# Performance work log

Measured on AMD Instinct MI355X. Metric: run time of the kernel, lower is better.

Reference implementation:

```python
import jax, jax.numpy as jnp
import numpy as np

EPS = 1e-5  # torch LayerNorm default

def layernorm(x, gamma, beta):
    mu = jnp.mean(x, axis=-1, keepdims=True)
    var = jnp.mean(jnp.square(x - mu), axis=-1, keepdims=True)
    return (x - mu) * jax.lax.rsqrt(var + EPS) * gamma + beta

def setup_inputs() -> dict:
    key = jax.random.key(0)
    ks = jax.random.split(key, 8)
    B, S, D = 4, 2048, 1024
    s = 1.0 / np.sqrt(D)  # torch Linear init scale
    return {
        "x": jax.random.normal(ks[0], (B, S, D), dtype=jnp.float32),
        "Wq": jax.random.uniform(ks[1], (D, D), jnp.float32, -s, s),
        "bq": jax.random.uniform(ks[2], (D,), jnp.float32, -s, s),
        "Wk": jax.random.uniform(ks[3], (D, D), jnp.float32, -s, s),
        "bk": jax.random.uniform(ks[4], (D,), jnp.float32, -s, s),
        "Wv": jax.random.uniform(ks[5], (D, D), jnp.float32, -s, s),
        "bv": jax.random.uniform(ks[6], (D,), jnp.float32, -s, s),
        "gamma": jnp.ones((D,), jnp.float32),
        "beta": jnp.zeros((D,), jnp.float32),
    }

def reference(x, Wq, bq, Wk, bk, Wv, bv, gamma, beta):
    # torch Linear: x @ W.T + b; shared LayerNorm applied to each projection
    q = layernorm(jnp.einsum('bsd,ed->bse', x, Wq) + bq, gamma, beta)
    k = layernorm(jnp.einsum('bsd,ed->bse', x, Wk) + bk, gamma, beta)
    v = layernorm(jnp.einsum('bsd,ed->bse', x, Wv) + bv, gamma, beta)
    att = jnp.einsum('bqd,bkd->bqk', q, k)  # no 1/sqrt(d) scaling in original
    att = jax.nn.softmax(att, axis=-1)
    # dropout is identity in eval mode (reference baseline)
    return jnp.einsum('bqk,bkd->bqd', att, v)
```

## Files before the change

kernel.cpp:

```cpp
#include <hip/hip_runtime.h>

typedef _Float16 f16;
typedef __attribute__((ext_vector_type(4))) _Float16 f16x4;
typedef __attribute__((ext_vector_type(8))) _Float16 f16x8;
typedef __attribute__((ext_vector_type(4))) float f32x4;

#define GLB_AS __attribute__((address_space(1)))
#define LDS_AS __attribute__((address_space(3)))

__device__ __forceinline__ void async_copy16(const void* g, void* l) {
  __builtin_amdgcn_global_load_lds((const GLB_AS void*)g, (LDS_AS void*)l, 16, 0, 0);
}

#define WAITVM(N) asm volatile("s_waitcnt vmcnt(" #N ")" ::: "memory")
#define WAITLGKM0() asm volatile("s_waitcnt lgkmcnt(0)" ::: "memory")

#define STAGE_A(t_) do {                                                     \
    const int _b = (t_) & 3; const long _k = (long)(t_) * 32;                \
    async_copy16(Ag + _k, &Ash[_b][sl]);                                     \
    if constexpr (IA == 2)                                                   \
      async_copy16(Ag + _k + 128l * lda, &Ash[_b][sl + 128 * 32]);           \
  } while (0)
#define STAGE_B(t_) do {                                                     \
    const int _b = (t_) & 3; const long _k = (long)(t_) * 32;                \
    async_copy16(Bg + _k, &Bsh[_b][sl]);                                     \
    if constexpr (IB == 2)                                                   \
      async_copy16(Bg + _k + 128l * ldb, &Bsh[_b][sl + 128 * 32]);           \
  } while (0)

template <int BM, int BN, typename OutT, int MODE, bool BIAS>
__global__ __launch_bounds__(512, 2) void gemm8p(
    const f16* __restrict__ A, const f16* __restrict__ B, OutT* __restrict__ C,
    int lda, int ldb, int ldc, int K, long sA, long sB, long sC,
    int tiles_x, int tiles_y,
    const float* __restrict__ b0, const float* __restrict__ b1,
    const float* __restrict__ b2)
{
  constexpr int BK = 32;
  constexpr int WM = BM / 2, WN = BN / 4;
  constexpr int RM = WM / 16, RN = WN / 16;
  constexpr int IA = BM / 128, IB = BN / 128;
  constexpr int IT = IA + IB;

  __shared__ __align__(16) f16 Ash[4][BM * BK];
  __shared__ __align__(16) f16 Bsh[4][BN * BK];

  int bx, by, bz;
  {
    const int n = blockIdx.x;
    if (MODE == 0) {
      by = n % tiles_y;
      const int r = n / tiles_y;
      bx = r % tiles_x;
      bz = r / tiles_x;
    } else {
      const int j = n & 7, i = n >> 3, th = tiles_y >> 1;
      bz = j >> 1;
      bx = i / th;
      by = (j & 1) * th + i % th;
    }
  }

  A += (long)bz * sA;
  B += (long)bz * sB;
  C += (long)bz * sC;

  const int tid  = threadIdx.x;
  const int wave = tid >> 6, lane = tid & 63;
  const int wr = wave >> 2, wc = wave & 3;
  const int m0 = by * BM, n0 = bx * BN;
  const int r16 = lane & 15, quad = lane >> 4;

  const int srow = wave * 16 + (lane >> 2);
  const int schunk = ((lane & 3) ^ ((lane >> 3) & 3)) * 8;
  const f16* Ag = A + (long)(m0 + srow) * lda + schunk;
  const f16* Bg = B + (long)(n0 + srow) * ldb + schunk;
  const int sl = (wave * 16) * BK;

  const int NT = K / BK;

  STAGE_A(0); STAGE_B(0);
  STAGE_A(1); STAGE_B(1);
  STAGE_A(2); STAGE_B(2);

  f32x4 acc[RM][RN] = {};

  const int rchunk = (quad ^ ((r16 >> 1) & 3)) * 8;
  const int rdA = (wr * WM + r16) * BK + rchunk;
  const int rdB = (wc * WN + r16) * BK + rchunk;

  for (int t = 0; t < NT; ++t) {
    if constexpr (IT == 4) {
      if (t < NT - 2) { WAITVM(8); } else if (t == NT - 2) { WAITVM(4); } else { WAITVM(0); }
    } else {
      if (t < NT - 2) { WAITVM(6); } else if (t == NT - 2) { WAITVM(3); } else { WAITVM(0); }
    }
    __builtin_amdgcn_s_barrier();

    const f16* As = Ash[t & 3];
    const f16* Bs = Bsh[t & 3];
    f16x8 af[4], bf[RN];

    if constexpr (RM == 8) {
#pragma unroll
      for (int j = 0; j < RN; j++) bf[j] = *(const f16x8*)&Bs[rdB + j * 16 * BK];
#pragma unroll
      for (int i = 0; i < 4; i++) af[i] = *(const f16x8*)&As[rdA + i * 16 * BK];
      if (t + 3 < NT) STAGE_A(t + 3);
      __builtin_amdgcn_s_barrier();
      WAITLGKM0();
      __builtin_amdgcn_sched_barrier(0);
      __builtin_amdgcn_s_setprio(1);
#pragma unroll
      for (int i = 0; i < 4; i++)
#pragma unroll
        for (int j = 0; j < RN; j++)
          acc[i][j] = __builtin_amdgcn_mfma_f32_16x16x32_f16(af[i], bf[j], acc[i][j], 0, 0, 0);
      __builtin_amdgcn_s_setprio(0);
      __builtin_amdgcn_sched_barrier(0);
      __builtin_amdgcn_s_barrier();
      f16x8 af1[4];
#pragma unroll
      for (int i = 0; i < 4; i++) af1[i] = *(const f16x8*)&As[rdA + (4 + i) * 16 * BK];
      if (t + 3 < NT) STAGE_B(t + 3);
      __builtin_amdgcn_s_barrier();
      WAITLGKM0();
      __builtin_amdgcn_sched_barrier(0);
      __builtin_amdgcn_s_setprio(1);
#pragma unroll
      for (int i = 0; i < 4; i++)
#pragma unroll
        for (int j = 0; j < RN; j++)
          acc[4 + i][j] = __builtin_amdgcn_mfma_f32_16x16x32_f16(af1[i], bf[j], acc[4 + i][j], 0, 0, 0);
      __builtin_amdgcn_s_setprio(0);
      __builtin_amdgcn_sched_barrier(0);
    } else {
#pragma unroll
      for (int i = 0; i < 4; i++) af[i] = *(const f16x8*)&As[rdA + i * 16 * BK];
#pragma unroll
      for (int j = 0; j < 2; j++) bf[j] = *(const f16x8*)&Bs[rdB + j * 16 * BK];
      if (t + 3 < NT) STAGE_A(t + 3);
      __builtin_amdgcn_s_barrier();
      WAITLGKM0();
      __builtin_amdgcn_sched_barrier(0);
      __builtin_amdgcn_s_setprio(1);
#pragma unroll
      for (int i = 0; i < 4; i++)
#pragma unroll
        for (int j = 0; j < 2; j++)
          acc[i][j] = __builtin_amdgcn_mfma_f32_16x16x32_f16(af[i], bf[j], acc[i][j], 0, 0, 0);
      __builtin_amdgcn_s_setprio(0);
      __builtin_amdgcn_sched_barrier(0);
      __builtin_amdgcn_s_barrier();
#pragma unroll
      for (int j = 2; j < 4; j++) bf[j] = *(const f16x8*)&Bs[rdB + j * 16 * BK];
      if (t + 3 < NT) STAGE_B(t + 3);
      __builtin_amdgcn_s_barrier();
      WAITLGKM0();
      __builtin_amdgcn_sched_barrier(0);
      __builtin_amdgcn_s_setprio(1);
#pragma unroll
      for (int i = 0; i < 4; i++)
#pragma unroll
        for (int j = 2; j < 4; j++)
          acc[i][j] = __builtin_amdgcn_mfma_f32_16x16x32_f16(af[i], bf[j], acc[i][j], 0, 0, 0);
      __builtin_amdgcn_s_setprio(0);
      __builtin_amdgcn_sched_barrier(0);
    }
  }

  float bias_j[RN];
#pragma unroll
  for (int j = 0; j < RN; j++) bias_j[j] = 0.f;
  if constexpr (BIAS) {
    const float* bias = (bz == 0) ? b0 : (bz == 1) ? b1 : b2;
#pragma unroll
    for (int j = 0; j < RN; j++) bias_j[j] = bias[n0 + wc * WN + j * 16 + r16];
  }
#pragma unroll
  for (int i = 0; i < RM; i++)
#pragma unroll
    for (int j = 0; j < RN; j++)
#pragma unroll
      for (int r = 0; r < 4; r++) {
        long row = m0 + wr * WM + i * 16 + quad * 4 + r;
        long col = n0 + wc * WN + j * 16 + r16;
        C[row * (long)ldc + col] = (OutT)(acc[i][j][r] + bias_j[j]);
      }
}

__global__ __launch_bounds__(256) void cast_all(
    const float* __restrict__ x, const float* __restrict__ Wq,
    const float* __restrict__ Wk, const float* __restrict__ Wv,
    f16* __restrict__ Xh, f16* __restrict__ Wh)
{
  const long off = (long)blockIdx.x * 1024 + threadIdx.x * 4;
  const float* src;
  f16* dst;
  if (off < 8388608L) {
    src = x + off;
    dst = Xh + off;
  } else {
    const long o = off - 8388608L;
    src = (o < 1048576L) ? Wq + o
        : (o < 2097152L) ? Wk + (o - 1048576L)
                         : Wv + (o - 2097152L);
    dst = Wh + o;
  }
  const float4 v = *(const float4*)src;
  f16x4 h;
  h.x = (f16)v.x; h.y = (f16)v.y; h.z = (f16)v.z; h.w = (f16)v.w;
  *(f16x4*)dst = h;
}

__global__ __launch_bounds__(256) void ln_kernel(
    f16* __restrict__ P, const float* __restrict__ gamma,
    const float* __restrict__ beta)
{
  f16* p = P + (long)blockIdx.y * 8388608 + (long)blockIdx.x * 1024;
  const int tid = threadIdx.x;
  const int e = tid * 4;

  f16x4 raw = *(const f16x4*)(p + e);
  float v0 = (float)raw.x, v1 = (float)raw.y;
  float v2 = (float)raw.z, v3 = (float)raw.w;
  float s  = v0 + v1 + v2 + v3;
  float s2 = v0 * v0 + v1 * v1 + v2 * v2 + v3 * v3;

#pragma unroll
  for (int off = 32; off > 0; off >>= 1) {
    s  += __shfl_down(s, off, 64);
    s2 += __shfl_down(s2, off, 64);
  }
  __shared__ float red[10];
  const int wave = tid >> 6, lane = tid & 63;
  if (lane == 0) { red[wave] = s; red[4 + wave] = s2; }
  __syncthreads();
  if (tid == 0) {
    red[8] = red[0] + red[1] + red[2] + red[3];
    red[9] = red[4] + red[5] + red[6] + red[7];
  }
  __syncthreads();
  const float mu   = red[8] * (1.f / 1024.f);
  const float var  = red[9] * (1.f / 1024.f) - mu * mu;
  const float rstd = rsqrtf(var + 1e-5f);

  float4 gg = *(const float4*)(gamma + e);
  float4 be = *(const float4*)(beta + e);
  f16x4 o;
  o.x = (f16)((v0 - mu) * rstd * gg.x + be.x);
  o.y = (f16)((v1 - mu) * rstd * gg.y + be.y);
  o.z = (f16)((v2 - mu) * rstd * gg.z + be.z);
  o.w = (f16)((v3 - mu) * rstd * gg.w + be.w);
  *(f16x4*)(p + e) = o;
}

__global__ __launch_bounds__(256) void transpose_kernel(const f16* __restrict__ V,
                                                        f16* __restrict__ Vt)
{
  const int S = 2048, D = 1024;
  const f16* v = V + (long)blockIdx.z * ((long)S * D);
  f16* vt = Vt + (long)blockIdx.z * ((long)D * S);
  __shared__ f16 tile[64][66];
  const int d0 = blockIdx.x * 64, j0 = blockIdx.y * 64;
  const int tx = threadIdx.x & 63, ty = threadIdx.x >> 6;
#pragma unroll
  for (int r = ty; r < 64; r += 4)
    tile[r][tx] = v[(long)(j0 + r) * D + d0 + tx];
  __syncthreads();
#pragma unroll
  for (int r = ty; r < 64; r += 4)
    vt[(long)(d0 + r) * S + j0 + tx] = tile[tx][r];
}

__global__ __launch_bounds__(256) void softmax_kernel(float* __restrict__ Sc)
{
  float* srow = Sc + (long)blockIdx.x * 2048;
  const int tid = threadIdx.x;
  float4 a = ((const float4*)srow)[tid];
  float4 b = ((const float4*)srow)[256 + tid];

  float m = fmaxf(fmaxf(fmaxf(a.x, a.y), fmaxf(a.z, a.w)),
                  fmaxf(fmaxf(b.x, b.y), fmaxf(b.z, b.w)));
#pragma unroll
  for (int off = 32; off > 0; off >>= 1) m = fmaxf(m, __shfl_down(m, off, 64));
  __shared__ float red[6];
  const int wave = tid >> 6, lane = tid & 63;
  if (lane == 0) red[wave] = m;
  __syncthreads();
  if (tid == 0) red[4] = fmaxf(fmaxf(red[0], red[1]), fmaxf(red[2], red[3]));
  __syncthreads();
  const float M = red[4];

  a.x = __expf(a.x - M); a.y = __expf(a.y - M);
  a.z = __expf(a.z - M); a.w = __expf(a.w - M);
  b.x = __expf(b.x - M); b.y = __expf(b.y - M);
  b.z = __expf(b.z - M); b.w = __expf(b.w - M);
  float s = a.x + a.y + a.z + a.w + b.x + b.y + b.z + b.w;
#pragma unroll
  for (int off = 32; off > 0; off >>= 1) s += __shfl_down(s, off, 64);
  if (lane == 0) red[wave] = s;
  __syncthreads();
  if (tid == 0) red[5] = red[0] + red[1] + red[2] + red[3];
  __syncthreads();
  const float inv = 1.0f / red[5];

  f16* orow = (f16*)srow;
  f16x4 oa, ob;
  oa.x = (f16)(a.x * inv); oa.y = (f16)(a.y * inv);
  oa.z = (f16)(a.z * inv); oa.w = (f16)(a.w * inv);
  ob.x = (f16)(b.x * inv); ob.y = (f16)(b.y * inv);
  ob.z = (f16)(b.z * inv); ob.w = (f16)(b.w * inv);
  ((f16x4*)orow)[tid]       = oa;
  ((f16x4*)orow)[256 + tid] = ob;
}

extern "C" void kernel_launch(void* const* d_in, const int* in_sizes, int n_in,
                              void* d_out, int out_size, void* d_ws, size_t ws_size,
                              hipStream_t stream)
{
  const float* x     = (const float*)d_in[0];
  const float* Wq    = (const float*)d_in[1];
  const float* bq    = (const float*)d_in[2];
  const float* Wk    = (const float*)d_in[3];
  const float* bk    = (const float*)d_in[4];
  const float* Wv    = (const float*)d_in[5];
  const float* bv    = (const float*)d_in[6];
  const float* gamma = (const float*)d_in[7];
  const float* beta  = (const float*)d_in[8];
  float* out = (float*)d_out;

  char* ws = (char*)d_ws;
  f16*   P  = (f16*)(ws);
  f16*   Vt = (f16*)(ws + (48u << 20));
  float* Sc = (float*)(ws + (64u << 20));
  f16*   Xh = (f16*)(ws + (64u << 20));
  f16*   Wh = (f16*)(ws + (80u << 20));

  cast_all<<<11264, 256, 0, stream>>>(x, Wq, Wk, Wv, Xh, Wh);

  gemm8p<128, 256, f16, 0, true><<<768, 512, 0, stream>>>(
      Xh, Wh, P, 1024, 1024, 1024, 1024, 0L, 1048576L, 8388608L,
      4, 64, bq, bk, bv);

  ln_kernel<<<dim3(8192, 3), 256, 0, stream>>>(P, gamma, beta);

  transpose_kernel<<<dim3(16, 32, 4), 256, 0, stream>>>(P + 2L * 8388608, Vt);

  gemm8p<256, 256, float, 1, false><<<256, 512, 0, stream>>>(
      P, P + 8388608, Sc, 1024, 1024, 2048, 1024, 2097152L, 2097152L, 4194304L,
      8, 8, nullptr, nullptr, nullptr);

  softmax_kernel<<<8192, 256, 0, stream>>>(Sc);

  gemm8p<128, 256, float, 1, false><<<256, 512, 0, stream>>>(
      (const f16*)Sc, Vt, out, 4096, 2048, 1024, 2048, 8388608L, 2097152L, 2097152L,
      4, 16, nullptr, nullptr, nullptr);
}
```

Before: 305.0 us.

## Restructure GEMM mainloop to double-buffered BK=64 with split half-tile staging

Replaces the 4-stage BK=32 ring buffer with a 2-stage buffer of 64-wide K tiles. Each tile is stored as two 32-wide halves, and each half is staged asynchronously while the other half is consumed. It also changes the LDS swizzle pattern to a three-way XOR to reduce bank conflicts, and restricts the template to BN=256. The intent is fewer barriers and waits per unit of K and better overlap of global-to-LDS copies with MFMA work. The cost is a shallower prefetch distance, a more complex wait-count schedule and a narrower supported configuration.

```diff
diff --git a/kernel.cpp b/kernel.cpp
--- a/kernel.cpp
+++ b/kernel.cpp
@@ -14,18 +14,20 @@
 
 #define WAITVM(N) asm volatile("s_waitcnt vmcnt(" #N ")" ::: "memory")
 #define WAITLGKM0() asm volatile("s_waitcnt lgkmcnt(0)" ::: "memory")
-
-#define STAGE_A(t_) do {                                                     \
-    const int _b = (t_) & 3; const long _k = (long)(t_) * 32;                \
-    async_copy16(Ag + _k, &Ash[_b][sl]);                                     \
-    if constexpr (IA == 2)                                                   \
-      async_copy16(Ag + _k + 128l * lda, &Ash[_b][sl + 128 * 32]);           \
+#define BAR() __builtin_amdgcn_s_barrier()
+#define SB0() __builtin_amdgcn_sched_barrier(0)
+
+#define STAGE_A(t_, kk_) do {                                                \
+    const long _k = (long)(t_) * 64 + (kk_) * 32;                            \
+    f16* _d = &Ash[(t_) & 1][kk_][w16 * 32];                                 \
+    async_copy16(Ag + _k, _d);                                               \
+    if constexpr (IA == 2) async_copy16(Ag + _k + 128l * lda, _d + 4096);    \
   } while (0)
-#define STAGE_B(t_) do {                                                     \
-    const int _b = (t_) & 3; const long _k = (long)(t_) * 32;                \
-    async_copy16(Bg + _k, &Bsh[_b][sl]);                                     \
-    if constexpr (IB == 2)                                                   \
-      async_copy16(Bg + _k + 128l * ldb, &Bsh[_b][sl + 128 * 32]);           \
+#define STAGE_B(t_, kk_) do {                                                \
+    const long _k = (long)(t_) * 64 + (kk_) * 32;                            \
+    f16* _d = &Bsh[(t_) & 1][kk_][w16 * 32];                                 \
+    async_copy16(Bg + _k, _d);                                               \
+    async_copy16(Bg + _k + 128l * ldb, _d + 4096);                           \
   } while (0)
 
 template <int BM, int BN, typename OutT, int MODE, bool BIAS>
@@ -36,14 +38,13 @@
     const float* __restrict__ b0, const float* __restrict__ b1,
     const float* __restrict__ b2)
 {
-  constexpr int BK = 32;
   constexpr int WM = BM / 2, WN = BN / 4;
   constexpr int RM = WM / 16, RN = WN / 16;
-  constexpr int IA = BM / 128, IB = BN / 128;
-  constexpr int IT = IA + IB;
-
-  __shared__ __align__(16) f16 Ash[4][BM * BK];
-  __shared__ __align__(16) f16 Bsh[4][BN * BK];
+  constexpr int IA = BM / 128;
+  static_assert(RN == 4 && BN == 256, "template assumes BN=256");
+
+  __shared__ __align__(16) f16 Ash[2][2][BM * 32];
+  __shared__ __align__(16) f16 Bsh[2][2][BN * 32];
 
   int bx, by, bz;
   {
@@ -70,102 +71,127 @@
   const int wr = wave >> 2, wc = wave & 3;
   const int m0 = by * BM, n0 = bx * BN;
   const int r16 = lane & 15, quad = lane >> 4;
-
-  const int srow = wave * 16 + (lane >> 2);
-  const int schunk = ((lane & 3) ^ ((lane >> 3) & 3)) * 8;
-  const f16* Ag = A + (long)(m0 + srow) * lda + schunk;
-  const f16* Bg = B + (long)(n0 + srow) * ldb + schunk;
-  const int sl = (wave * 16) * BK;
-
-  const int NT = K / BK;
-
-  STAGE_A(0); STAGE_B(0);
-  STAGE_A(1); STAGE_B(1);
-  STAGE_A(2); STAGE_B(2);
+  const int w16 = wave * 16;
+
+  const int cg8 = (((lane & 3) ^ ((lane >> 2) & 3) ^ ((lane >> 4) & 3)) * 8);
+  const f16* Ag = A + (long)(m0 + w16 + (lane >> 2)) * lda + cg8;
+  const f16* Bg = B + (long)(n0 + w16 + (lane >> 2)) * ldb + cg8;
+
+  const int NT = K / 64;
+
+  STAGE_A(0, 0); STAGE_B(0, 0);
+  STAGE_A(0, 1); STAGE_B(0, 1);
+  STAGE_A(1, 0); STAGE_B(1, 0);
 
   f32x4 acc[RM][RN] = {};
 
-  const int rchunk = (quad ^ ((r16 >> 1) & 3)) * 8;
-  const int rdA = (wr * WM + r16) * BK + rchunk;
-  const int rdB = (wc * WN + r16) * BK + rchunk;
+  const int rc  = (quad ^ ((r16 ^ (r16 >> 2)) & 3)) * 8;
+  const int rdA = (wr * WM + r16) * 32 + rc;
+  const int rdB = (wc * WN + r16) * 32 + rc;
+
+  if constexpr (RM == 8) { WAITVM(8); } else { WAITVM(6); }
+  BAR();
 
   for (int t = 0; t < NT; ++t) {
-    if constexpr (IT == 4) {
-      if (t < NT - 2) { WAITVM(8); } else if (t == NT - 2) { WAITVM(4); } else { WAITVM(0); }
+    const int bp = t & 1;
+    const f16* A0 = &Ash[bp][0][0];
+    const f16* A1 = &Ash[bp][1][0];
+    const f16* B0 = &Bsh[bp][0][0];
+    const f16* B1 = &Bsh[bp][1][0];
+    f16x8 af[4], bf[4];
+
+    if constexpr (RM == 4) {
+#pragma unroll
+      for (int i = 0; i < 4; i++) af[i] = *(const f16x8*)&A0[rdA + i * 512];
+#pragma unroll
+      for (int j = 0; j < 4; j++) bf[j] = *(const f16x8*)&B0[rdB + j * 512];
+      if (t + 1 < NT) { STAGE_A(t + 1, 1); STAGE_B(t + 1, 1); }
+      BAR();
+      WAITLGKM0(); SB0();
+      __builtin_amdgcn_s_setprio(1);
+#pragma unroll
+      for (int i = 0; i < 4; i++)
+#pragma unroll
+        for (int j = 0; j < 4; j++)
+          acc[i][j] = __builtin_amdgcn_mfma_f32_16x16x32_f16(af[i], bf[j], acc[i][j], 0, 0, 0);
+      __builtin_amdgcn_s_setprio(0); SB0();
+      if (t < NT - 1) { WAITVM(6); } else { WAITVM(0); }
+      BAR();
+#pragma unroll
+      for (int i = 0; i < 4; i++) af[i] = *(const f16x8*)&A1[rdA + i * 512];
+#pragma unroll
+      for (int j = 0; j < 4; j++) bf[j] = *(const f16x8*)&B1[rdB + j * 512];
+      if (t + 2 < NT) { STAGE_A(t + 2, 0); STAGE_B(t + 2, 0); }
+      BAR();
+      WAITLGKM0(); SB0();
+      __builtin_amdgcn_s_setprio(1);
+#pragma unroll
+      for (int i = 0; i < 4; i++)
+#pragma unroll
+        for (int j = 0; j < 4; j++)
+          acc[i][j] = __builtin_amdgcn_mfma_f32_16x16x32_f16(af[i], bf[j], acc[i][j], 0, 0, 0);
+      __builtin_amdgcn_s_setprio(0); SB0();
+      if (t < NT - 2) { WAITVM(6); } else if (t == NT - 2) { WAITVM(3); } else { WAITVM(0); }
+      BAR();
     } else {
-      if (t < NT - 2) { WAITVM(6); } else if (t == NT - 2) { WAITVM(3); } else { WAITVM(0); }
-    }
-    __builtin_amdgcn_s_barrier();
-
-    const f16* As = Ash[t & 3];
-    const f16* Bs = Bsh[t & 3];
-    f16x8 af[4], bf[RN];
-
-    if constexpr (RM == 8) {
-#pragma unroll
-      for (int j = 0; j < RN; j++) bf[j] = *(const f16x8*)&Bs[rdB + j * 16 * BK];
-#pragma unroll
-      for (int i = 0; i < 4; i++) af[i] = *(const f16x8*)&As[rdA + i * 16 * BK];
-      if (t + 3 < NT) STAGE_A(t + 3);
-      __builtin_amdgcn_s_barrier();
-      WAITLGKM0();
-      __builtin_amdgcn_sched_barrier(0);
-      __builtin_amdgcn_s_setprio(1);
-#pragma unroll
-      for (int i = 0; i < 4; i++)
-#pragma unroll
-        for (int j = 0; j < RN; j++)
+#pragma unroll
+      for (int i = 0; i < 4; i++) af[i] = *(const f16x8*)&A0[rdA + i * 512];
+#pragma unroll
+      for (int j = 0; j < 4; j++) bf[j] = *(const f16x8*)&B0[rdB + j * 512];
+      if (t + 1 < NT) STAGE_A(t + 1, 1);
+      BAR();
+      WAITLGKM0(); SB0();
+      __builtin_amdgcn_s_setprio(1);
+#pragma unroll
+      for (int i = 0; i < 4; i++)
+#pragma unroll
+        for (int j = 0; j < 4; j++)
           acc[i][j] = __builtin_amdgcn_mfma_f32_16x16x32_f16(af[i], bf[j], acc[i][j], 0, 0, 0);
-      __builtin_amdgcn_s_setprio(0);
-      __builtin_amdgcn_sched_barrier(0);
-      __builtin_amdgcn_s_barrier();
-      f16x8 af1[4];
-#pragma unroll
-      for (int i = 0; i < 4; i++) af1[i] = *(const f16x8*)&As[rdA + (4 + i) * 16 * BK];
-      if (t + 3 < NT) STAGE_B(t + 3);
-      __builtin_amdgcn_s_barrier();
-      WAITLGKM0();
-      __builtin_amdgcn_sched_barrier(0);
-      __builtin_amdgcn_s_setprio(1);
-#pragma unroll
-      for (int i = 0; i < 4; i++)
-#pragma unroll
-        for (int j = 0; j < RN; j++)
-          acc[4 + i][j] = __builtin_amdgcn_mfma_f32_16x16x32_f16(af1[i], bf[j], acc[4 + i][j], 0, 0, 0);
-      __builtin_amdgcn_s_setprio(0);
-      __builtin_amdgcn_sched_barrier(0);
-    } else {
-#pragma unroll
-      for (int i = 0; i < 4; i++) af[i] = *(const f16x8*)&As[rdA + i * 16 * BK];
-#pragma unroll
-      for (int j = 0; j < 2; j++) bf[j] = *(const f16x8*)&Bs[rdB + j * 16 * BK];
-      if (t + 3 < NT) STAGE_A(t + 3);
-      __builtin_amdgcn_s_barrier();
-      WAITLGKM0();
-      __builtin_amdgcn_sched_barrier(0);
-      __builtin_amdgcn_s_setprio(1);
-#pragma unroll
-      for (int i = 0; i < 4; i++)
-#pragma unroll
-        for (int j = 0; j < 2; j++)
+      __builtin_amdgcn_s_setprio(0); SB0();
+      BAR();
+#pragma unroll
+      for (int i = 0; i < 4; i++) af[i] = *(const f16x8*)&A0[rdA + (4 + i) * 512];
+      if (t + 1 < NT) STAGE_B(t + 1, 1);
+      BAR();
+      WAITLGKM0(); SB0();
+      __builtin_amdgcn_s_setprio(1);
+#pragma unroll
+      for (int i = 0; i < 4; i++)
+#pragma unroll
+        for (int j = 0; j < 4; j++)
+          acc[4 + i][j] = __builtin_amdgcn_mfma_f32_16x16x32_f16(af[i], bf[j], acc[4 + i][j], 0, 0, 0);
+      __builtin_amdgcn_s_setprio(0); SB0();
+      if (t < NT - 1) { WAITVM(6); } else { WAITVM(0); }
+      BAR();
+#pragma unroll
+      for (int i = 0; i < 4; i++) af[i] = *(const f16x8*)&A1[rdA + i * 512];
+#pragma unroll
+      for (int j = 0; j < 4; j++) bf[j] = *(const f16x8*)&B1[rdB + j * 512];
+      if (t + 2 < NT) STAGE_A(t + 2, 0);
+      BAR();
+      WAITLGKM0(); SB0();
+      __builtin_amdgcn_s_setprio(1);
+#pragma unroll
+      for (int i = 0; i < 4; i++)
+#pragma unroll
+        for (int j = 0; j < 4; j++)
           acc[i][j] = __builtin_amdgcn_mfma_f32_16x16x32_f16(af[i], bf[j], acc[i][j], 0, 0, 0);
-      __builtin_amdgcn_s_setprio(0);
-      __builtin_amdgcn_sched_barrier(0);
-      __builtin_amdgcn_s_barrier();
-#pragma unroll
-      for (int j = 2; j < 4; j++) bf[j] = *(const f16x8*)&Bs[rdB + j * 16 * BK];
-      if (t + 3 < NT) STAGE_B(t + 3);
-      __builtin_amdgcn_s_barrier();
-      WAITLGKM0();
-      __builtin_amdgcn_sched_barrier(0);
-      __builtin_amdgcn_s_setprio(1);
-#pragma unroll
-      for (int i = 0; i < 4; i++)
-#pragma unroll
-        for (int j = 2; j < 4; j++)
-          acc[i][j] = __builtin_amdgcn_mfma_f32_16x16x32_f16(af[i], bf[j], acc[i][j], 0, 0, 0);
-      __builtin_amdgcn_s_setprio(0);
-      __builtin_amdgcn_sched_barrier(0);
+      __builtin_amdgcn_s_setprio(0); SB0();
+      BAR();
+#pragma unroll
+      for (int i = 0; i < 4; i++) af[i] = *(const f16x8*)&A1[rdA + (4 + i) * 512];
+      if (t + 2 < NT) STAGE_B(t + 2, 0);
+      BAR();
+      WAITLGKM0(); SB0();
+      __builtin_amdgcn_s_setprio(1);
+#pragma unroll
+      for (int i = 0; i < 4; i++)
+#pragma unroll
+        for (int j = 0; j < 4; j++)
+          acc[4 + i][j] = __builtin_amdgcn_mfma_f32_16x16x32_f16(af[i], bf[j], acc[4 + i][j], 0, 0, 0);
+      __builtin_amdgcn_s_setprio(0); SB0();
+      if (t < NT - 2) { WAITVM(6); } else if (t == NT - 2) { WAITVM(4); } else { WAITVM(0); }
+      BAR();
     }
   }
 
```

Result: no change. 300.2 us (-1.6%).
